# Performance work log

Hardware: AMD Instinct MI355X
Metric: run time of the kernel (lower is better)

## Reference

```python
import jax, jax.numpy as jnp
import numpy as np

EP = 65536      # entity pairs (segments)
L = 8           # rows per span
N = EP * L      # total logit rows
C = 97          # relation classes (class 0 = threshold class)
BIG = 1e30


def setup_inputs() -> dict:
    key = jax.random.key(0)
    k1, k2 = jax.random.split(key)
    logits = jax.random.normal(k1, (N, C), dtype=jnp.float32)
    labels = (jax.random.uniform(k2, (EP, C)) < 0.03).astype(jnp.float32)
    starts = jnp.arange(EP, dtype=jnp.int32) * L
    pos = jnp.stack([starts, starts + L], axis=1)  # contiguous [st, en) spans
    return {"logits": logits, "labels": labels, "pos": pos}


def reference(logits, labels, pos):
    ep = pos.shape[0]
    n = logits.shape[0]
    # contiguous spans cover [0, N): row i belongs to segment j with end_j > i
    seg_ids = jnp.searchsorted(pos[:, 1], jnp.arange(n, dtype=pos.dtype), side="right")
    # ragged per-span max-reduction (single fused segment-max)
    e_logits = jax.ops.segment_max(logits, seg_ids, num_segments=ep)  # [EP, C]
    # threshold column taken from the first ep rows of raw logits
    e_logits = e_logits.at[:, 0].set(logits[:ep, 0])

    th_label = jnp.zeros_like(labels).at[:, 0].set(1.0)
    labels = labels.at[:, 0].set(0.0)
    p_mask = labels + th_label
    n_mask = 1.0 - labels

    loss1 = -(jax.nn.log_softmax(e_logits - (1.0 - p_mask) * BIG, axis=-1) * labels).sum(1)
    loss2 = -(jax.nn.log_softmax(e_logits - (1.0 - n_mask) * BIG, axis=-1) * th_label).sum(1)
    return (loss1 + loss2).mean()
```

## Files before the change

### kernel.cpp

```cpp
#include <hip/hip_runtime.h>
#include <math.h>

#define EP 65536
#define C 97
#define L 8
#define WAVES 4
#define ITERS 8
#define SEG_PER_BLOCK (WAVES * ITERS)
#define NBLOCKS (EP / SEG_PER_BLOCK)
#define SEG_FLOATS (L * C)

typedef float f4 __attribute__((ext_vector_type(4)));

__device__ __forceinline__ void wsum3(float& a, float& b, float& c) {
#pragma unroll
    for (int o = 32; o > 0; o >>= 1) {
        a += __shfl_xor(a, o, 64);
        b += __shfl_xor(b, o, 64);
        c += __shfl_xor(c, o, 64);
    }
}

__global__ __launch_bounds__(256) void atloss_main(
        const float* __restrict__ logits,
        const float* __restrict__ labels,
        const int*   __restrict__ pos,
        float*       __restrict__ partials) {
    const int tid  = threadIdx.x;
    const int w    = tid >> 6;
    const int lane = tid & 63;
    const int jbase = blockIdx.x * SEG_PER_BLOCK + w * ITERS;

    __shared__ float s_log[WAVES * SEG_FLOATS];
    __shared__ float s_loss[WAVES];
    float* seg_s = s_log + w * SEG_FLOATS;
    f4*    s4    = (f4*)seg_s;

    const int  c0   = lane;
    const int  c1   = lane + 64;
    const bool has1 = (c1 < C);

    int st_l = 0;
    if (lane < ITERS) st_l = pos[2 * (jbase + lane)];

    int st_s[ITERS];
#pragma unroll
    for (int k = 0; k < ITERS; ++k)
        st_s[k] = __builtin_amdgcn_readlane(st_l, k);

    const f4* g4 = (const f4*)(logits + (size_t)st_s[0] * C);
    f4 A0 = __builtin_nontemporal_load(g4 + lane);
    f4 A1 = __builtin_nontemporal_load(g4 + lane + 64);
    f4 A2 = __builtin_nontemporal_load(g4 + lane + 128);
    f4 A3 = (f4){0.f, 0.f, 0.f, 0.f};
    if (lane < 2) A3 = __builtin_nontemporal_load(g4 + 192 + lane);
    const size_t lbb = (size_t)jbase * C;
    float LB0 = __builtin_nontemporal_load(labels + lbb + c0);
    float LB1 = has1 ? __builtin_nontemporal_load(labels + lbb + c1) : 0.0f;
    float ETH = logits[(size_t)jbase * C];

    float wloss = 0.0f;

#pragma unroll
    for (int it = 0; it < ITERS; ++it) {
        const f4 B0 = A0, B1 = A1, B2 = A2, B3 = A3;
        const float lb0 = LB0, lb1 = LB1, eth = ETH;
        if (it + 1 < ITERS) {
            const int j1 = jbase + it + 1;
            const f4* g4n = (const f4*)(logits + (size_t)st_s[it + 1] * C);
            A0 = __builtin_nontemporal_load(g4n + lane);
            A1 = __builtin_nontemporal_load(g4n + lane + 64);
            A2 = __builtin_nontemporal_load(g4n + lane + 128);
            if (lane < 2) A3 = __builtin_nontemporal_load(g4n + 192 + lane);
            const size_t lbn = (size_t)j1 * C;
            LB0 = __builtin_nontemporal_load(labels + lbn + c0);
            LB1 = has1 ? __builtin_nontemporal_load(labels + lbn + c1) : 0.0f;
            ETH = logits[(size_t)j1 * C];
        }

        s4[lane] = B0; s4[lane + 64] = B1; s4[lane + 128] = B2;
        if (lane < 2) s4[192 + lane] = B3;

        float e0, e1 = -INFINITY;
        {
            const float m01 = fmaxf(seg_s[0 * C + c0], seg_s[1 * C + c0]);
            const float m23 = fmaxf(seg_s[2 * C + c0], seg_s[3 * C + c0]);
            const float m45 = fmaxf(seg_s[4 * C + c0], seg_s[5 * C + c0]);
            const float m67 = fmaxf(seg_s[6 * C + c0], seg_s[7 * C + c0]);
            e0 = fmaxf(fmaxf(m01, m23), fmaxf(m45, m67));
        }
        if (has1) {
            const float m01 = fmaxf(seg_s[0 * C + c1], seg_s[1 * C + c1]);
            const float m23 = fmaxf(seg_s[2 * C + c1], seg_s[3 * C + c1]);
            const float m45 = fmaxf(seg_s[4 * C + c1], seg_s[5 * C + c1]);
            const float m67 = fmaxf(seg_s[6 * C + c1], seg_s[7 * C + c1]);
            e1 = fmaxf(fmaxf(m01, m23), fmaxf(m45, m67));
        }
        if (lane == 0) e0 = eth;

        const bool p0 = (lane > 0) && (lb0 > 0.5f);
        const bool p1 = has1 && (lb1 > 0.5f);

        const float npos = (float)(__popcll(__ballot(p0)) +
                                   __popcll(__ballot(p1)));

        const float x0 = __expf(e0);
        const float x1 = has1 ? __expf(e1) : 0.0f;

        float s_all  = x0 + x1;
        float sp_pos = (p0 ? x0 : 0.0f) + (p1 ? x1 : 0.0f);
        float spos   = (p0 ? e0 : 0.0f) + (p1 ? e1 : 0.0f);
        wsum3(s_all, sp_pos, spos);

        const float x_th = __expf(eth);
        const float sp = x_th + sp_pos;
        const float sn = s_all - sp_pos;
        wloss += npos * __logf(sp) - spos + (__logf(sn) - eth);
    }

    if (lane == 0) s_loss[w] = wloss;
    __syncthreads();
    if (tid == 0) {
        partials[blockIdx.x] = s_loss[0] + s_loss[1] + s_loss[2] + s_loss[3];
    }
}

__global__ __launch_bounds__(256) void atloss_reduce(
        const float* __restrict__ partials, int n, float* __restrict__ out) {
    __shared__ double sh[256];
    double acc = 0.0;
    for (int i = threadIdx.x; i < n; i += 256) acc += (double)partials[i];
    sh[threadIdx.x] = acc;
    __syncthreads();
    for (int s = 128; s > 0; s >>= 1) {
        if (threadIdx.x < s) sh[threadIdx.x] += sh[threadIdx.x + s];
        __syncthreads();
    }
    if (threadIdx.x == 0) out[0] = (float)(sh[0] / (double)EP);
}

extern "C" void kernel_launch(void* const* d_in, const int* in_sizes, int n_in,
                              void* d_out, int out_size, void* d_ws, size_t ws_size,
                              hipStream_t stream) {
    const float* logits = (const float*)d_in[0];
    const float* labels = (const float*)d_in[1];
    const int*   pos    = (const int*)d_in[2];
    float* out      = (float*)d_out;
    float* partials = (float*)d_ws;

    atloss_main<<<NBLOCKS, 256, 0, stream>>>(logits, labels, pos, partials);
    atloss_reduce<<<1, 256, 0, stream>>>(partials, NBLOCKS, out);
}
```

Before: 46.40 us.

## Load segment rows directly into registers, drop LDS staging and defer spos reduction

Replaces the per-wave LDS staging of each 8x97 segment (vector loads, then strided LDS reads for the max) with direct per-lane scalar loads of each row's two columns into registers, computing the segment max in registers. Labels and threshold logits for all eight segments are preloaded up front, with the labels packed into bitmasks. The per-segment positive-logit sum is accumulated per lane and reduced once at the end, so each iteration needs two wave reductions instead of three. Launch bounds now request higher occupancy. In exchange the kernel issues many more scalar global loads instead of 16-byte vector loads, and holds more registers for the prefetched rows.

```diff
diff --git a/kernel.cpp b/kernel.cpp
--- a/kernel.cpp
+++ b/kernel.cpp
@@ -8,20 +8,21 @@
 #define ITERS 8
 #define SEG_PER_BLOCK (WAVES * ITERS)
 #define NBLOCKS (EP / SEG_PER_BLOCK)
-#define SEG_FLOATS (L * C)
 
-typedef float f4 __attribute__((ext_vector_type(4)));
-
-__device__ __forceinline__ void wsum3(float& a, float& b, float& c) {
+__device__ __forceinline__ void wsum2(float& a, float& b) {
 #pragma unroll
     for (int o = 32; o > 0; o >>= 1) {
         a += __shfl_xor(a, o, 64);
         b += __shfl_xor(b, o, 64);
-        c += __shfl_xor(c, o, 64);
     }
 }
+__device__ __forceinline__ float wsum(float v) {
+#pragma unroll
+    for (int o = 32; o > 0; o >>= 1) v += __shfl_xor(v, o, 64);
+    return v;
+}
 
-__global__ __launch_bounds__(256) void atloss_main(
+__global__ __launch_bounds__(256, 8) void atloss_main(
         const float* __restrict__ logits,
         const float* __restrict__ labels,
         const int*   __restrict__ pos,
@@ -31,10 +32,7 @@
     const int lane = tid & 63;
     const int jbase = blockIdx.x * SEG_PER_BLOCK + w * ITERS;
 
-    __shared__ float s_log[WAVES * SEG_FLOATS];
     __shared__ float s_loss[WAVES];
-    float* seg_s = s_log + w * SEG_FLOATS;
-    f4*    s4    = (f4*)seg_s;
 
     const int  c0   = lane;
     const int  c1   = lane + 64;
@@ -42,65 +40,65 @@
 
     int st_l = 0;
     if (lane < ITERS) st_l = pos[2 * (jbase + lane)];
-
     int st_s[ITERS];
 #pragma unroll
     for (int k = 0; k < ITERS; ++k)
         st_s[k] = __builtin_amdgcn_readlane(st_l, k);
 
-    const f4* g4 = (const f4*)(logits + (size_t)st_s[0] * C);
-    f4 A0 = __builtin_nontemporal_load(g4 + lane);
-    f4 A1 = __builtin_nontemporal_load(g4 + lane + 64);
-    f4 A2 = __builtin_nontemporal_load(g4 + lane + 128);
-    f4 A3 = (f4){0.f, 0.f, 0.f, 0.f};
-    if (lane < 2) A3 = __builtin_nontemporal_load(g4 + 192 + lane);
-    const size_t lbb = (size_t)jbase * C;
-    float LB0 = __builtin_nontemporal_load(labels + lbb + c0);
-    float LB1 = has1 ? __builtin_nontemporal_load(labels + lbb + c1) : 0.0f;
-    float ETH = logits[(size_t)jbase * C];
+    unsigned pm0 = 0, pm1 = 0;
+#pragma unroll
+    for (int k = 0; k < ITERS; ++k) {
+        const size_t lb = (size_t)(jbase + k) * C;
+        const float l0 = __builtin_nontemporal_load(labels + lb + c0);
+        const float l1 = has1 ? __builtin_nontemporal_load(labels + lb + c1)
+                              : 0.0f;
+        pm0 |= (unsigned)((lane > 0) && (l0 > 0.5f)) << k;
+        pm1 |= (unsigned)(has1 && (l1 > 0.5f)) << k;
+    }
 
-    float wloss = 0.0f;
+    float eth_s[ITERS];
+#pragma unroll
+    for (int k = 0; k < ITERS; ++k)
+        eth_s[k] = __int_as_float(__builtin_amdgcn_readfirstlane(
+            __float_as_int(logits[(size_t)(jbase + k) * C])));
+
+    float a0[L], a1[L];
+    {
+        const float* rb = logits + (size_t)st_s[0] * C;
+#pragma unroll
+        for (int r = 0; r < L; ++r) {
+            a0[r] = __builtin_nontemporal_load(rb + r * C + c0);
+            a1[r] = has1 ? __builtin_nontemporal_load(rb + r * C + c1)
+                         : -INFINITY;
+        }
+    }
+
+    float acc_uni = 0.0f, acc_spos = 0.0f;
 
 #pragma unroll
     for (int it = 0; it < ITERS; ++it) {
-        const f4 B0 = A0, B1 = A1, B2 = A2, B3 = A3;
-        const float lb0 = LB0, lb1 = LB1, eth = ETH;
+        float v0[L], v1[L];
+#pragma unroll
+        for (int r = 0; r < L; ++r) { v0[r] = a0[r]; v1[r] = a1[r]; }
         if (it + 1 < ITERS) {
-            const int j1 = jbase + it + 1;
-            const f4* g4n = (const f4*)(logits + (size_t)st_s[it + 1] * C);
-            A0 = __builtin_nontemporal_load(g4n + lane);
-            A1 = __builtin_nontemporal_load(g4n + lane + 64);
-            A2 = __builtin_nontemporal_load(g4n + lane + 128);
-            if (lane < 2) A3 = __builtin_nontemporal_load(g4n + 192 + lane);
-            const size_t lbn = (size_t)j1 * C;
-            LB0 = __builtin_nontemporal_load(labels + lbn + c0);
-            LB1 = has1 ? __builtin_nontemporal_load(labels + lbn + c1) : 0.0f;
-            ETH = logits[(size_t)j1 * C];
+            const float* rb = logits + (size_t)st_s[it + 1] * C;
+#pragma unroll
+            for (int r = 0; r < L; ++r) {
+                a0[r] = __builtin_nontemporal_load(rb + r * C + c0);
+                a1[r] = has1 ? __builtin_nontemporal_load(rb + r * C + c1)
+                             : -INFINITY;
+            }
         }
+        const float eth = eth_s[it];
 
-        s4[lane] = B0; s4[lane + 64] = B1; s4[lane + 128] = B2;
-        if (lane < 2) s4[192 + lane] = B3;
-
-        float e0, e1 = -INFINITY;
-        {
-            const float m01 = fmaxf(seg_s[0 * C + c0], seg_s[1 * C + c0]);
-            const float m23 = fmaxf(seg_s[2 * C + c0], seg_s[3 * C + c0]);
-            const float m45 = fmaxf(seg_s[4 * C + c0], seg_s[5 * C + c0]);
-            const float m67 = fmaxf(seg_s[6 * C + c0], seg_s[7 * C + c0]);
-            e0 = fmaxf(fmaxf(m01, m23), fmaxf(m45, m67));
-        }
-        if (has1) {
-            const float m01 = fmaxf(seg_s[0 * C + c1], seg_s[1 * C + c1]);
-            const float m23 = fmaxf(seg_s[2 * C + c1], seg_s[3 * C + c1]);
-            const float m45 = fmaxf(seg_s[4 * C + c1], seg_s[5 * C + c1]);
-            const float m67 = fmaxf(seg_s[6 * C + c1], seg_s[7 * C + c1]);
-            e1 = fmaxf(fmaxf(m01, m23), fmaxf(m45, m67));
-        }
+        float e0 = fmaxf(fmaxf(fmaxf(v0[0], v0[1]), fmaxf(v0[2], v0[3])),
+                         fmaxf(fmaxf(v0[4], v0[5]), fmaxf(v0[6], v0[7])));
+        float e1 = fmaxf(fmaxf(fmaxf(v1[0], v1[1]), fmaxf(v1[2], v1[3])),
+                         fmaxf(fmaxf(v1[4], v1[5]), fmaxf(v1[6], v1[7])));
         if (lane == 0) e0 = eth;
 
-        const bool p0 = (lane > 0) && (lb0 > 0.5f);
-        const bool p1 = has1 && (lb1 > 0.5f);
-
+        const bool p0 = (pm0 >> it) & 1u;
+        const bool p1 = (pm1 >> it) & 1u;
         const float npos = (float)(__popcll(__ballot(p0)) +
                                    __popcll(__ballot(p1)));
 
@@ -109,14 +107,15 @@
 
         float s_all  = x0 + x1;
         float sp_pos = (p0 ? x0 : 0.0f) + (p1 ? x1 : 0.0f);
-        float spos   = (p0 ? e0 : 0.0f) + (p1 ? e1 : 0.0f);
-        wsum3(s_all, sp_pos, spos);
+        wsum2(s_all, sp_pos);
 
-        const float x_th = __expf(eth);
-        const float sp = x_th + sp_pos;
+        const float sp = __expf(eth) + sp_pos;
         const float sn = s_all - sp_pos;
-        wloss += npos * __logf(sp) - spos + (__logf(sn) - eth);
+        acc_uni  += npos * __logf(sp) + (__logf(sn) - eth);
+        acc_spos += (p0 ? e0 : 0.0f) + (p1 ? e1 : 0.0f);
     }
+
+    const float wloss = acc_uni - wsum(acc_spos);
 
     if (lane == 0) s_loss[w] = wloss;
     __syncthreads();
```

New measurement: 76.48 us. 64.8% more time.
